# Kernel optimization log

Measured on AMD Instinct MI355X. Metric: run time of the kernel, lower is better.

## Reference

```python
import jax, jax.numpy as jnp
import numpy as np

N, D, K = 32768, 512, 8192   # nodes, embedding_dim, num_embeddings
COMMITMENT_COST = 0.25
EPS = 1e-12


def _l2norm(v, axis=-1):
    # matches torch.nn.functional.normalize(p=2): divide by clamped norm
    n = jnp.linalg.norm(v, axis=axis, keepdims=True)
    return v / jnp.maximum(n, EPS)


def setup_inputs() -> dict:
    key = jax.random.key(0)
    kx, kw = jax.random.split(key)
    x = jax.random.normal(kx, (N, D), dtype=jnp.float32)
    codebook = jax.random.normal(kw, (K, D), dtype=jnp.float32)  # nn.Embedding weight
    return {"x": x, "codebook": codebook}


def reference(x, codebook):
    # VectorQuantizer.forward
    xn = _l2norm(x)                      # [N, D]
    wn = _l2norm(codebook)               # [K, D]  (normalize(W.t(), dim=0).T == normalize(W, dim=-1))
    dist = (jnp.sum(xn * xn, axis=-1, keepdims=True)
            + jnp.sum(wn * wn, axis=1)
            - 2.0 * (xn @ wn.T))
    encoding_indices = jnp.argmin(dist, axis=1)          # [N]
    quantized = _l2norm(codebook[encoding_indices])      # gather + renormalize, [N, D]

    q_latent_loss = jnp.mean((quantized - jax.lax.stop_gradient(xn)) ** 2)
    e_latent_loss = jnp.mean((xn - jax.lax.stop_gradient(quantized)) ** 2)
    loss = q_latent_loss + COMMITMENT_COST * e_latent_loss

    # straight-through estimator
    quantized_st = xn + jax.lax.stop_gradient(quantized - xn)
    return quantized_st, loss, encoding_indices
```

## Files before the change

### kernel.cpp

```cpp
#include <hip/hip_runtime.h>

#define N_ROWS 32768
#define DIM    512
#define K_CODES 8192
#define BM 128
#define BN 128
#define BK 64
#define NB (K_CODES / BN)
#define MARGIN 3e-3f

typedef short s16x8 __attribute__((ext_vector_type(8)));
typedef float f32x4 __attribute__((ext_vector_type(4)));
typedef unsigned long long u64;

__device__ __forceinline__ unsigned short f2bf(float f) {
  unsigned int u = __float_as_uint(f);
  u = (u + 0x7fffu + ((u >> 16) & 1u)) >> 16;
  return (unsigned short)u;
}

__device__ __forceinline__ unsigned int ordf(float f) {
  unsigned int u = __float_as_uint(f);
  return (u & 0x80000000u) ? ~u : (u | 0x80000000u);
}
__device__ __forceinline__ float unordf(unsigned int o) {
  return (o & 0x80000000u) ? __uint_as_float(o ^ 0x80000000u) : __uint_as_float(~o);
}

__device__ __forceinline__ void gload_lds16(const void* g, void* l) {
  __builtin_amdgcn_global_load_lds(
      (const __attribute__((address_space(1))) void*)g,
      (__attribute__((address_space(3))) void*)l,
      16, 0, 0);
}

__global__ void prep_all(const float* __restrict__ W, const float* __restrict__ X,
                         unsigned short* __restrict__ wn16, unsigned short* __restrict__ xn16,
                         float* __restrict__ wnorm, float* __restrict__ wn2,
                         float* __restrict__ xnorm) {
  int b = blockIdx.x;
  bool isW = b < (K_CODES / 4);
  int row = (isW ? b : b - K_CODES / 4) * 4 + (threadIdx.x >> 6);
  int l = threadIdx.x & 63;
  const float* src = isW ? W : X;
  const float4* p = (const float4*)&src[(size_t)row * DIM + l * 8];
  float4 v0 = p[0], v1 = p[1];
  float ss = v0.x * v0.x + v0.y * v0.y + v0.z * v0.z + v0.w * v0.w
           + v1.x * v1.x + v1.y * v1.y + v1.z * v1.z + v1.w * v1.w;
#pragma unroll
  for (int o = 32; o; o >>= 1) ss += __shfl_xor(ss, o);
  float nrm = fmaxf(sqrtf(ss), 1e-12f);
  float q[8];
  q[0] = v0.x / nrm; q[1] = v0.y / nrm; q[2] = v0.z / nrm; q[3] = v0.w / nrm;
  q[4] = v1.x / nrm; q[5] = v1.y / nrm; q[6] = v1.z / nrm; q[7] = v1.w / nrm;
  s16x8 bv;
#pragma unroll
  for (int j = 0; j < 8; j++) bv[j] = (short)f2bf(q[j]);
  unsigned short* dst = isW ? wn16 : xn16;
  *(s16x8*)&dst[(size_t)row * DIM + l * 8] = bv;
  if (isW) {
    float s2 = q[0]*q[0] + q[1]*q[1] + q[2]*q[2] + q[3]*q[3]
             + q[4]*q[4] + q[5]*q[5] + q[6]*q[6] + q[7]*q[7];
#pragma unroll
    for (int o = 32; o; o >>= 1) s2 += __shfl_xor(s2, o);
    if (l == 0) { wnorm[row] = nrm; wn2[row] = s2; }
  } else {
    if (l == 0) xnorm[row] = nrm;
  }
}

__global__ __launch_bounds__(256, 4) void gemm_top2(
    const unsigned short* __restrict__ xn16, const unsigned short* __restrict__ wn16,
    float* __restrict__ pv, int* __restrict__ pi) {
  union SMem {
    struct { unsigned short A[BM * BK]; unsigned short B[BN * BK]; } st;
    uint4 ep[64 * 33];
  };
  __shared__ SMem sm;
  int bx = blockIdx.x;
  int by = blockIdx.y;
  int t = threadIdx.x;
  int w = t >> 6, l = t & 63;
  int wr = w >> 1, wc = w & 1;
  int rr = l & 15, hi = l >> 4;
  f32x4 acc[4][4] = {};

  int srow = t >> 3;
  int sg = (t & 7) ^ (srow & 7);
  const unsigned short* aP = xn16 + (size_t)by * BM * DIM + (size_t)srow * DIM + sg * 8;
  const unsigned short* bP = wn16 + (size_t)bx * BN * DIM + (size_t)srow * DIM + sg * 8;

  int aB0 = (wr * 64 + rr) * BK + ((hi ^ (rr & 7)) * 8);
  int bB0 = (wc * 64 + rr) * BK + ((hi ^ (rr & 7)) * 8);

  for (int k0 = 0; k0 < DIM; k0 += BK) {
#pragma unroll
    for (int i = 0; i < 4; i++) {
      gload_lds16(aP + i * 16384, &sm.st.A[(i * 256 + t) * 8]);
      gload_lds16(bP + i * 16384, &sm.st.B[(i * 256 + t) * 8]);
    }
    aP += BK; bP += BK;
    __syncthreads();

    s16x8 aF[4], bF[4];
#pragma unroll
    for (int m = 0; m < 4; m++) aF[m] = *(const s16x8*)&sm.st.A[aB0 + m * 1024];
#pragma unroll
    for (int n = 0; n < 4; n++) bF[n] = *(const s16x8*)&sm.st.B[bB0 + n * 1024];
#pragma unroll
    for (int m = 0; m < 4; m++)
#pragma unroll
      for (int n = 0; n < 4; n++)
        acc[m][n] = __builtin_amdgcn_mfma_f32_16x16x32_bf16(aF[m], bF[n], acc[m][n], 0, 0, 0);
#pragma unroll
    for (int m = 0; m < 4; m++) aF[m] = *(const s16x8*)&sm.st.A[(aB0 ^ 32) + m * 1024];
#pragma unroll
    for (int n = 0; n < 4; n++) bF[n] = *(const s16x8*)&sm.st.B[(bB0 ^ 32) + n * 1024];
#pragma unroll
    for (int m = 0; m < 4; m++)
#pragma unroll
      for (int n = 0; n < 4; n++)
        acc[m][n] = __builtin_amdgcn_mfma_f32_16x16x32_bf16(aF[m], bF[n], acc[m][n], 0, 0, 0);
    __syncthreads();
  }

  int wcbase = wc * 64;

  auto scan_write = [&]() {
#pragma unroll
    for (int m = 0; m < 4; m++)
#pragma unroll
      for (int r = 0; r < 4; r++) {
        float v0 = acc[m][0][r], v1 = acc[m][1][r], v2 = acc[m][2][r], v3 = acc[m][3][r];
        float a1, a2, d1, d2, t1, t2; int i1, i2, j1, j2, u1, u2;
        if (v1 > v0) { a1 = v1; i1 = 1; a2 = v0; i2 = 0; } else { a1 = v0; i1 = 0; a2 = v1; i2 = 1; }
        if (v3 > v2) { d1 = v3; j1 = 3; d2 = v2; j2 = 2; } else { d1 = v2; j1 = 2; d2 = v3; j2 = 3; }
        if (a1 >= d1) { t1 = a1; u1 = i1; if (d1 > a2) { t2 = d1; u2 = j1; } else { t2 = a2; u2 = i2; } }
        else          { t1 = d1; u1 = j1; if (a1 >= d2) { t2 = a1; u2 = i1; } else { t2 = d2; u2 = j2; } }
        int col1 = wcbase + u1 * 16 + rr, col2 = wcbase + u2 * 16 + rr;
        u64 k1 = ((u64)ordf(t1) << 32) | (unsigned)(~col1);
        u64 k2 = ((u64)ordf(t2) << 32) | (unsigned)(~col2);
        int rloc = m * 16 + hi * 4 + r;
        int e = wc * 16 + rr;
        int slot = (e + rloc) & 31;
        sm.ep[rloc * 33 + slot] =
            make_uint4((unsigned)k1, (unsigned)(k1 >> 32), (unsigned)k2, (unsigned)(k2 >> 32));
      }
  };

  auto finalize_store = [&](int pass) {
    u64 K1 = 0, K2 = 0;
#pragma unroll 4
    for (int e = 0; e < 32; e++) {
      uint4 qq = sm.ep[t * 33 + ((e + t) & 31)];
      u64 e1 = ((u64)qq.y << 32) | qq.x;
      u64 e2 = ((u64)qq.w << 32) | qq.z;
      if (e1 > K1) { K2 = (K1 > e2) ? K1 : e2; K1 = e1; }
      else if (e1 > K2) { K2 = e1; }
    }
    int rowl = pass * 64 + t;
    size_t rowg = (size_t)by * BM + rowl;
    float f1 = unordf((unsigned)(K1 >> 32));
    float f2 = unordf((unsigned)(K2 >> 32));
    int c1 = (int)(~(unsigned)K1);
    int c2 = (int)(~(unsigned)K2);
    pv[(size_t)(bx * 2 + 0) * N_ROWS + rowg] = f1;
    pv[(size_t)(bx * 2 + 1) * N_ROWS + rowg] = f2;
    pi[(size_t)(bx * 2 + 0) * N_ROWS + rowg] = bx * BN + c1;
    pi[(size_t)(bx * 2 + 1) * N_ROWS + rowg] = bx * BN + c2;
  };

  if (wr == 0) scan_write();
  __syncthreads();
  if (t < 64) finalize_store(0);
  __syncthreads();
  if (wr == 1) scan_write();
  __syncthreads();
  if (t < 64) finalize_store(1);
}

__global__ void collapse(const float* __restrict__ pv, const int* __restrict__ pi,
                         int* __restrict__ cand) {
  int r = blockIdx.x * 256 + threadIdx.x;
  float mx = -1e30f; int be = 0;
#pragma unroll 8
  for (int e = 0; e < 2 * NB; e++) {
    float v = pv[(size_t)e * N_ROWS + r];
    if (v > mx) { mx = v; be = e; }
  }
  float thr = mx - MARGIN;
  cand[r * 8 + 1] = pi[(size_t)be * N_ROWS + r];
  int cnt = 1;
  for (int e = 0; e < 2 * NB; e++) {
    if (e == be) continue;
    float v = pv[(size_t)e * N_ROWS + r];
    if (v >= thr && cnt < 7) { cand[r * 8 + 1 + cnt] = pi[(size_t)e * N_ROWS + r]; cnt++; }
  }
  cand[r * 8] = cnt;
}

__global__ void reduce_rescore(
    const float* __restrict__ X, const float* __restrict__ W,
    const float* __restrict__ xnorm, const float* __restrict__ wnorm,
    const float* __restrict__ wn2, const int* __restrict__ cand,
    float* __restrict__ out, float* __restrict__ partial, float* __restrict__ outIdx) {
  int row = blockIdx.x * 4 + (threadIdx.x >> 6);
  int l = threadIdx.x & 63;

  float xnrm = xnorm[row];
  const float4* xp = (const float4*)&X[(size_t)row * DIM + l * 8];
  float4 a0 = xp[0], a1 = xp[1];
  float xq[8];
  xq[0] = a0.x / xnrm; xq[1] = a0.y / xnrm; xq[2] = a0.z / xnrm; xq[3] = a0.w / xnrm;
  xq[4] = a1.x / xnrm; xq[5] = a1.y / xnrm; xq[6] = a1.z / xnrm; xq[7] = a1.w / xnrm;

  int cnt = cand[row * 8];
  float bestDist = 1e30f; int bestIdx = 0x7fffffff;
  for (int ci = 0; ci < cnt; ci++) {
    int c = cand[row * 8 + 1 + ci];
    float wnr = wnorm[c];
    const float4* wp = (const float4*)&W[(size_t)c * DIM + l * 8];
    float4 w0 = wp[0], w1 = wp[1];
    float d = xq[0] * (w0.x / wnr) + xq[1] * (w0.y / wnr)
            + xq[2] * (w0.z / wnr) + xq[3] * (w0.w / wnr)
            + xq[4] * (w1.x / wnr) + xq[5] * (w1.y / wnr)
            + xq[6] * (w1.z / wnr) + xq[7] * (w1.w / wnr);
#pragma unroll
    for (int o = 32; o; o >>= 1) d += __shfl_xor(d, o);
    float dist = wn2[c] - 2.0f * d;
    if (dist < bestDist || (dist == bestDist && c < bestIdx)) { bestDist = dist; bestIdx = c; }
  }

  int c = bestIdx;
  float wnr = wnorm[c];
  const float4* wp = (const float4*)&W[(size_t)c * DIM + l * 8];
  float4 w0 = wp[0], w1 = wp[1];
  float q[8];
  q[0] = w0.x / wnr; q[1] = w0.y / wnr; q[2] = w0.z / wnr; q[3] = w0.w / wnr;
  q[4] = w1.x / wnr; q[5] = w1.y / wnr; q[6] = w1.z / wnr; q[7] = w1.w / wnr;
  float4 o0, o1;
  o0.x = xq[0] + (q[0] - xq[0]); o0.y = xq[1] + (q[1] - xq[1]);
  o0.z = xq[2] + (q[2] - xq[2]); o0.w = xq[3] + (q[3] - xq[3]);
  o1.x = xq[4] + (q[4] - xq[4]); o1.y = xq[5] + (q[5] - xq[5]);
  o1.z = xq[6] + (q[6] - xq[6]); o1.w = xq[7] + (q[7] - xq[7]);
  float4* op = (float4*)&out[(size_t)row * DIM + l * 8];
  op[0] = o0; op[1] = o1;
  float ssum = 0.f;
#pragma unroll
  for (int j = 0; j < 8; j++) { float df = q[j] - xq[j]; ssum += df * df; }
#pragma unroll
  for (int o = 32; o; o >>= 1) ssum += __shfl_xor(ssum, o);
  if (l == 0) { partial[row] = ssum; outIdx[row] = (float)c; }
}

__global__ void reduce_loss(const float* __restrict__ partial, float* __restrict__ accum) {
  int i = blockIdx.x * 256 + threadIdx.x;
  float s = partial[i];
#pragma unroll
  for (int o = 32; o; o >>= 1) s += __shfl_xor(s, o);
  if ((threadIdx.x & 63) == 0) atomicAdd(accum, s);
}

__global__ void write_loss(const float* __restrict__ accum, float* __restrict__ out) {
  out[0] = (float)(1.25 * (double)accum[0] / (double)((size_t)N_ROWS * DIM));
}

extern "C" void kernel_launch(void* const* d_in, const int* in_sizes, int n_in,
                              void* d_out, int out_size, void* d_ws, size_t ws_size,
                              hipStream_t stream) {
  const float* x = (const float*)d_in[0];
  const float* W = (const float*)d_in[1];
  float* out = (float*)d_out;
  char* ws = (char*)d_ws;

  unsigned short* wn16 = (unsigned short*)(ws);
  unsigned short* xn16 = (unsigned short*)(ws + 8388608);
  float* wnorm = (float*)(ws + 41943040);
  float* wn2   = (float*)(ws + 41975808);
  float* xnorm = (float*)(ws + 42008576);
  float* pv    = (float*)(ws + 42139648);
  int*   pi    = (int*)  (ws + 58916864);
  float* accum = (float*)(ws + 75694080);
  float* partial = (float*)(ws + 8388608);
  int*   cand    = (int*)  (ws + 8519680);

  hipMemsetAsync(accum, 0, sizeof(float), stream);
  prep_all<<<K_CODES / 4 + N_ROWS / 4, 256, 0, stream>>>(W, x, wn16, xn16, wnorm, wn2, xnorm);
  dim3 grid(NB, N_ROWS / BM);
  gemm_top2<<<grid, 256, 0, stream>>>(xn16, wn16, pv, pi);
  collapse<<<N_ROWS / 256, 256, 0, stream>>>(pv, pi, cand);
  reduce_rescore<<<N_ROWS / 4, 256, 0, stream>>>(
      x, W, xnorm, wnorm, wn2, cand, out, partial,
      out + (size_t)N_ROWS * DIM + 1);
  reduce_loss<<<N_ROWS / 256, 256, 0, stream>>>(partial, accum);
  write_loss<<<1, 1, 0, stream>>>(accum, out + (size_t)N_ROWS * DIM);
}
```

Before: 591.4 us.

## Enlarge GEMM tiles to 256x256 with 512 threads and XCD-aware block swizzle

```diff
diff --git a/kernel.cpp b/kernel.cpp
--- a/kernel.cpp
+++ b/kernel.cpp
@@ -3,8 +3,8 @@
 #define N_ROWS 32768
 #define DIM    512
 #define K_CODES 8192
-#define BM 128
-#define BN 128
+#define BM 256
+#define BN 256
 #define BK 64
 #define NB (K_CODES / BN)
 #define MARGIN 3e-3f
@@ -32,6 +32,11 @@
       (const __attribute__((address_space(1))) void*)g,
       (__attribute__((address_space(3))) void*)l,
       16, 0, 0);
+}
+
+__device__ __forceinline__ void kmerge(u64& K1, u64& K2, u64 e1, u64 e2) {
+  if (e1 > K1) { K2 = (K1 > e2) ? K1 : e2; K1 = e1; }
+  else if (e1 > K2) { K2 = e1; }
 }
 
 __global__ void prep_all(const float* __restrict__ W, const float* __restrict__ X,
@@ -69,114 +74,106 @@
   }
 }
 
-__global__ __launch_bounds__(256, 4) void gemm_top2(
+__global__ __launch_bounds__(512, 2) void gemm_top2(
     const unsigned short* __restrict__ xn16, const unsigned short* __restrict__ wn16,
     float* __restrict__ pv, int* __restrict__ pi) {
   union SMem {
     struct { unsigned short A[BM * BK]; unsigned short B[BN * BK]; } st;
-    uint4 ep[64 * 33];
+    uint4 ep[64 * 65];
   };
   __shared__ SMem sm;
-  int bx = blockIdx.x;
-  int by = blockIdx.y;
+  int wg = blockIdx.x;
+  int virt = (wg & 7) * 512 + (wg >> 3);
+  int bx = virt >> 7;
+  int by = virt & 127;
   int t = threadIdx.x;
   int w = t >> 6, l = t & 63;
-  int wr = w >> 1, wc = w & 1;
+  int wr = w >> 2, wc = w & 3;
   int rr = l & 15, hi = l >> 4;
-  f32x4 acc[4][4] = {};
+  f32x4 acc[8][4] = {};
 
   int srow = t >> 3;
   int sg = (t & 7) ^ (srow & 7);
   const unsigned short* aP = xn16 + (size_t)by * BM * DIM + (size_t)srow * DIM + sg * 8;
   const unsigned short* bP = wn16 + (size_t)bx * BN * DIM + (size_t)srow * DIM + sg * 8;
 
-  int aB0 = (wr * 64 + rr) * BK + ((hi ^ (rr & 7)) * 8);
+  int aB0 = (wr * 128 + rr) * BK + ((hi ^ (rr & 7)) * 8);
   int bB0 = (wc * 64 + rr) * BK + ((hi ^ (rr & 7)) * 8);
 
   for (int k0 = 0; k0 < DIM; k0 += BK) {
 #pragma unroll
     for (int i = 0; i < 4; i++) {
-      gload_lds16(aP + i * 16384, &sm.st.A[(i * 256 + t) * 8]);
-      gload_lds16(bP + i * 16384, &sm.st.B[(i * 256 + t) * 8]);
+      gload_lds16(aP + (size_t)i * 64 * DIM, &sm.st.A[(i * 512 + t) * 8]);
+      gload_lds16(bP + (size_t)i * 64 * DIM, &sm.st.B[(i * 512 + t) * 8]);
     }
     aP += BK; bP += BK;
     __syncthreads();
 
-    s16x8 aF[4], bF[4];
-#pragma unroll
-    for (int m = 0; m < 4; m++) aF[m] = *(const s16x8*)&sm.st.A[aB0 + m * 1024];
-#pragma unroll
-    for (int n = 0; n < 4; n++) bF[n] = *(const s16x8*)&sm.st.B[bB0 + n * 1024];
-#pragma unroll
-    for (int m = 0; m < 4; m++)
-#pragma unroll
-      for (int n = 0; n < 4; n++)
-        acc[m][n] = __builtin_amdgcn_mfma_f32_16x16x32_bf16(aF[m], bF[n], acc[m][n], 0, 0, 0);
-#pragma unroll
-    for (int m = 0; m < 4; m++) aF[m] = *(const s16x8*)&sm.st.A[(aB0 ^ 32) + m * 1024];
-#pragma unroll
-    for (int n = 0; n < 4; n++) bF[n] = *(const s16x8*)&sm.st.B[(bB0 ^ 32) + n * 1024];
-#pragma unroll
-    for (int m = 0; m < 4; m++)
-#pragma unroll
-      for (int n = 0; n < 4; n++)
-        acc[m][n] = __builtin_amdgcn_mfma_f32_16x16x32_bf16(aF[m], bF[n], acc[m][n], 0, 0, 0);
+    s16x8 aF[8], bF[4];
+#pragma unroll
+    for (int ks = 0; ks < 2; ks++) {
+      int x = ks * 32;
+#pragma unroll
+      for (int m = 0; m < 8; m++) aF[m] = *(const s16x8*)&sm.st.A[(aB0 + m * 1024) ^ x];
+#pragma unroll
+      for (int n = 0; n < 4; n++) bF[n] = *(const s16x8*)&sm.st.B[(bB0 + n * 1024) ^ x];
+#pragma unroll
+      for (int m = 0; m < 8; m++)
+#pragma unroll
+        for (int n = 0; n < 4; n++)
+          acc[m][n] = __builtin_amdgcn_mfma_f32_16x16x32_bf16(aF[m], bF[n], acc[m][n], 0, 0, 0);
+    }
     __syncthreads();
   }
 
   int wcbase = wc * 64;
-
-  auto scan_write = [&]() {
-#pragma unroll
-    for (int m = 0; m < 4; m++)
-#pragma unroll
-      for (int r = 0; r < 4; r++) {
-        float v0 = acc[m][0][r], v1 = acc[m][1][r], v2 = acc[m][2][r], v3 = acc[m][3][r];
-        float a1, a2, d1, d2, t1, t2; int i1, i2, j1, j2, u1, u2;
-        if (v1 > v0) { a1 = v1; i1 = 1; a2 = v0; i2 = 0; } else { a1 = v0; i1 = 0; a2 = v1; i2 = 1; }
-        if (v3 > v2) { d1 = v3; j1 = 3; d2 = v2; j2 = 2; } else { d1 = v2; j1 = 2; d2 = v3; j2 = 3; }
-        if (a1 >= d1) { t1 = a1; u1 = i1; if (d1 > a2) { t2 = d1; u2 = j1; } else { t2 = a2; u2 = i2; } }
-        else          { t1 = d1; u1 = j1; if (a1 >= d2) { t2 = a1; u2 = i1; } else { t2 = d2; u2 = j2; } }
-        int col1 = wcbase + u1 * 16 + rr, col2 = wcbase + u2 * 16 + rr;
-        u64 k1 = ((u64)ordf(t1) << 32) | (unsigned)(~col1);
-        u64 k2 = ((u64)ordf(t2) << 32) | (unsigned)(~col2);
-        int rloc = m * 16 + hi * 4 + r;
-        int e = wc * 16 + rr;
-        int slot = (e + rloc) & 31;
-        sm.ep[rloc * 33 + slot] =
-            make_uint4((unsigned)k1, (unsigned)(k1 >> 32), (unsigned)k2, (unsigned)(k2 >> 32));
+#pragma unroll
+  for (int P = 0; P < 4; P++) {
+    if (wr == (P >> 1)) {
+      const int mlo = (P & 1) * 4;
+#pragma unroll
+      for (int mm = 0; mm < 4; mm++) {
+#pragma unroll
+        for (int r = 0; r < 4; r++) {
+          float v0 = acc[mlo + mm][0][r], v1 = acc[mlo + mm][1][r];
+          float v2 = acc[mlo + mm][2][r], v3 = acc[mlo + mm][3][r];
+          float a1, a2, d1, d2, t1, t2; int i1, i2, j1, j2, u1, u2;
+          if (v1 > v0) { a1 = v1; i1 = 1; a2 = v0; i2 = 0; } else { a1 = v0; i1 = 0; a2 = v1; i2 = 1; }
+          if (v3 > v2) { d1 = v3; j1 = 3; d2 = v2; j2 = 2; } else { d1 = v2; j1 = 2; d2 = v3; j2 = 3; }
+          if (a1 >= d1) { t1 = a1; u1 = i1; if (d1 > a2) { t2 = d1; u2 = j1; } else { t2 = a2; u2 = i2; } }
+          else          { t1 = d1; u1 = j1; if (a1 >= d2) { t2 = a1; u2 = i1; } else { t2 = d2; u2 = j2; } }
+          int col1 = wcbase + u1 * 16 + rr, col2 = wcbase + u2 * 16 + rr;
+          u64 k1 = ((u64)ordf(t1) << 32) | (unsigned)(~col1);
+          u64 k2 = ((u64)ordf(t2) << 32) | (unsigned)(~col2);
+          int row64 = mm * 16 + hi * 4 + r;
+          sm.ep[row64 * 65 + wc * 16 + rr] =
+              make_uint4((unsigned)k1, (unsigned)(k1 >> 32), (unsigned)k2, (unsigned)(k2 >> 32));
+        }
       }
-  };
-
-  auto finalize_store = [&](int pass) {
-    u64 K1 = 0, K2 = 0;
-#pragma unroll 4
-    for (int e = 0; e < 32; e++) {
-      uint4 qq = sm.ep[t * 33 + ((e + t) & 31)];
-      u64 e1 = ((u64)qq.y << 32) | qq.x;
-      u64 e2 = ((u64)qq.w << 32) | qq.z;
-      if (e1 > K1) { K2 = (K1 > e2) ? K1 : e2; K1 = e1; }
-      else if (e1 > K2) { K2 = e1; }
-    }
-    int rowl = pass * 64 + t;
-    size_t rowg = (size_t)by * BM + rowl;
-    float f1 = unordf((unsigned)(K1 >> 32));
-    float f2 = unordf((unsigned)(K2 >> 32));
-    int c1 = (int)(~(unsigned)K1);
-    int c2 = (int)(~(unsigned)K2);
-    pv[(size_t)(bx * 2 + 0) * N_ROWS + rowg] = f1;
-    pv[(size_t)(bx * 2 + 1) * N_ROWS + rowg] = f2;
-    pi[(size_t)(bx * 2 + 0) * N_ROWS + rowg] = bx * BN + c1;
-    pi[(size_t)(bx * 2 + 1) * N_ROWS + rowg] = bx * BN + c2;
-  };
-
-  if (wr == 0) scan_write();
-  __syncthreads();
-  if (t < 64) finalize_store(0);
-  __syncthreads();
-  if (wr == 1) scan_write();
-  __syncthreads();
-  if (t < 64) finalize_store(1);
+    }
+    __syncthreads();
+    if (t < 128) {
+      int row64 = t >> 1, seg = t & 1;
+      u64 K1 = 0, K2 = 0;
+      for (int j = 0; j < 32; j++) {
+        uint4 q = sm.ep[row64 * 65 + seg * 32 + j];
+        u64 e1 = ((u64)q.y << 32) | q.x;
+        u64 e2 = ((u64)q.w << 32) | q.z;
+        kmerge(K1, K2, e1, e2);
+      }
+      unsigned o1l = __shfl_xor((unsigned)K1, 1), o1h = __shfl_xor((unsigned)(K1 >> 32), 1);
+      unsigned o2l = __shfl_xor((unsigned)K2, 1), o2h = __shfl_xor((unsigned)(K2 >> 32), 1);
+      kmerge(K1, K2, ((u64)o1h << 32) | o1l, ((u64)o2h << 32) | o2l);
+      if (seg == 0) {
+        size_t rowg = (size_t)by * BM + P * 64 + row64;
+        pv[(size_t)(bx * 2 + 0) * N_ROWS + rowg] = unordf((unsigned)(K1 >> 32));
+        pv[(size_t)(bx * 2 + 1) * N_ROWS + rowg] = unordf((unsigned)(K2 >> 32));
+        pi[(size_t)(bx * 2 + 0) * N_ROWS + rowg] = bx * BN + (int)(~(unsigned)K1);
+        pi[(size_t)(bx * 2 + 1) * N_ROWS + rowg] = bx * BN + (int)(~(unsigned)K2);
+      }
+    }
+    __syncthreads();
+  }
 }
 
 __global__ void collapse(const float* __restrict__ pv, const int* __restrict__ pi,
@@ -286,8 +283,7 @@
 
   hipMemsetAsync(accum, 0, sizeof(float), stream);
   prep_all<<<K_CODES / 4 + N_ROWS / 4, 256, 0, stream>>>(W, x, wn16, xn16, wnorm, wn2, xnorm);
-  dim3 grid(NB, N_ROWS / BM);
-  gemm_top2<<<grid, 256, 0, stream>>>(xn16, wn16, pv, pi);
+  gemm_top2<<<(K_CODES / BN) * (N_ROWS / BM), 512, 0, stream>>>(xn16, wn16, pv, pi);
   collapse<<<N_ROWS / 256, 256, 0, stream>>>(pv, pi, cand);
   reduce_rescore<<<N_ROWS / 4, 256, 0, stream>>>(
       x, W, xnorm, wnorm, wn2, cand, out, partial,
```

Measured after the change: 1.225 ms. +107.2%, slower.
